# Optimization experiments

Measured on AMD Instinct MI355X. Metric: run time of the kernel, lower is better.

Reference implementation:

```python
import jax, jax.numpy as jnp
import numpy as np

N, M, DIM, OUT_DIM = 50000, 512, 256, 256
NEG = -1e9


def setup_inputs() -> dict:
    key = jax.random.key(0)
    k1, k2, k3, k4, k5, k6 = jax.random.split(key, 6)
    node_features = jax.random.normal(k1, (N, DIM), dtype=jnp.float32)
    # each node assigned to one molecule (sorted segment ids)
    mol_ids = jnp.sort(jax.random.randint(k2, (N,), 0, M))
    mol_node_matrix = (mol_ids[None, :] == jnp.arange(M)[:, None]).astype(jnp.float32)  # [M, N]
    mol_node_mask = jnp.where(mol_node_matrix > 0, 0.0, NEG).astype(jnp.float32)  # [M, N]
    # Linear params (PyTorch-style uniform init)
    bound = 1.0 / np.sqrt(DIM)
    W_attend = jax.random.uniform(k3, (DIM, OUT_DIM), minval=-bound, maxval=bound, dtype=jnp.float32)
    b_attend = jax.random.uniform(k4, (OUT_DIM,), minval=-bound, maxval=bound, dtype=jnp.float32)
    w_align = jax.random.uniform(k5, (DIM, 1), minval=-bound, maxval=bound, dtype=jnp.float32)
    b_align = jax.random.uniform(k6, (1,), minval=-bound, maxval=bound, dtype=jnp.float32)
    return {"node_features": node_features, "mol_node_matrix": mol_node_matrix,
            "mol_node_mask": mol_node_mask, "W_attend": W_attend, "b_attend": b_attend,
            "w_align": w_align, "b_align": b_align}


def reference(node_features, mol_node_matrix, mol_node_mask, W_attend, b_attend, w_align, b_align):
    # h = LeakyReLU(attend(x)) : [N, out_dim]
    h = jax.nn.leaky_relu(node_features @ W_attend + b_attend, negative_slope=0.01)
    # a = align(x) : [N]  (dropout p=0 -> identity)
    a = (node_features @ w_align + b_align)[:, 0]
    # mol_node_matrix @ diag(a) == mol_node_matrix * a[None, :]  (same math, no NxN diag)
    logits = mol_node_matrix * a[None, :] + mol_node_mask  # [M, N]
    mol_node_weight = jax.nn.softmax(logits, axis=1)
    return mol_node_weight @ h, mol_node_weight
```

## Files before the change

kernel.cpp:

```cpp
#include <hip/hip_runtime.h>
#include <cstdint>
#include <cstddef>

#define N_NODES 50000
#define M_MOLS  512
#define DIMK    256
#define ODIM    256

#define NCH   99
#define CW    32
#define NSAMP (NCH * CW)
#define NGAP  (NCH - 1)

#define NB_WPACK 32
#define K0_GRID  (NCH + NB_WPACK)

#define NB_ALIGN 1563
#define K1_GRID  (NGAP + NCH + 1 + NB_ALIGN)

#define POOL_BLOCKS 512
#define WPB   4
#define QPB   3125
#define NB_WRITE (M_MOLS * WPB)
#define K2_GRID  (POOL_BLOCKS + NB_WRITE)
#define NF4   (N_NODES / 4)
#define A_CAP 1024

typedef float  f32x4  __attribute__((ext_vector_type(4)));
typedef __bf16 bf16x8 __attribute__((ext_vector_type(8)));

static __device__ __forceinline__ short f2bf(float f) {
  unsigned u = __builtin_bit_cast(unsigned, f);
  u = u + 0x7fffu + ((u >> 16) & 1u);
  return (short)(u >> 16);
}

static __device__ __forceinline__ int chunk_base(int c) {
  return (c < NCH - 1) ? c * 512 : (N_NODES - CW);
}

__global__ __launch_bounds__(256) void k_prep(
    const float* __restrict__ mat, const float* __restrict__ W,
    int* __restrict__ smolid, int4* __restrict__ wp) {
  int b = blockIdx.x, t = threadIdx.x;
  if (b < NCH) {
    int base = chunk_base(b);
    int cp = (t & 15) * 2;
    int rg = t >> 4;
    int idx = -1, idy = -1;
    const float* p0 = mat + (size_t)(rg * 32) * N_NODES + base + cp;
#pragma unroll 16
    for (int r = 0; r < 32; r++) {
      float2 v = *(const float2*)(p0 + (size_t)r * N_NODES);
      if (v.x != 0.f) idx = rg * 32 + r;
      if (v.y != 0.f) idy = rg * 32 + r;
    }
    __shared__ int sm[16][32];
    sm[rg][cp] = idx; sm[rg][cp + 1] = idy;
    __syncthreads();
    if (t < 32) {
      int best = -1;
#pragma unroll
      for (int g = 0; g < 16; g++) best = max(best, sm[g][t]);
      smolid[b * CW + t] = best;
    }
  } else {
    int g  = (b - NCH) * 256 + t;
    int l  = g & 63;
    int Ju = g >> 6;
    int J  = Ju >> 3, u = Ju & 7;
    int j  = J * 16 + (l & 15);
    int k0 = u * 32 + (l >> 4) * 8;
    short sv[8];
#pragma unroll
    for (int i = 0; i < 8; i++) sv[i] = f2bf(W[(size_t)(k0 + i) * ODIM + j]);
    wp[Ju * 64 + l] = *(int4*)sv;
  }
}

__global__ __launch_bounds__(256) void k_bal(
    const float* __restrict__ x, const float* __restrict__ mat,
    const float* __restrict__ wa, const float* __restrict__ ba,
    const int* __restrict__ smolid, int* __restrict__ strt,
    float* __restrict__ a) {
  int b = blockIdx.x, t = threadIdx.x;
  if (b < NGAP) {
    int p  = chunk_base(b) + CW - 1;
    int q  = chunk_base(b + 1);
    int ag = smolid[b * CW + CW - 1];
    int bg = smolid[(b + 1) * CW];
    if (bg == ag) return;
    int Wd = q - p;
    int nr = bg - ag;
    __shared__ int f1[512];
    int wave = t >> 6, l = t & 63;
    for (int rr = wave; rr < nr; rr += 4) {
      const float* rp = mat + (size_t)(ag + 1 + rr) * N_NODES + p + 1;
      int mn = 0x7fffffff;
      for (int i = l; i < Wd; i += 64)
        if (rp[i] != 0.f) { mn = i; break; }
#pragma unroll
      for (int o = 1; o < 64; o <<= 1) mn = min(mn, __shfl_xor(mn, o));
      if (l == 0) f1[rr] = mn;
    }
    __syncthreads();
    if (t == 0) {
      int run = 0x7fffffff;
      for (int rr = nr - 1; rr >= 0; rr--) {
        run = min(run, f1[rr]);
        strt[ag + 1 + rr] = p + 1 + run;
      }
    }
  } else if (b < NGAP + NCH) {
    int cc = b - NGAP;
    if (t >= 1 && t < CW) {
      int prev = smolid[cc * CW + t - 1], cur = smolid[cc * CW + t];
      int col = chunk_base(cc) + t;
      for (int m = prev + 1; m <= cur; m++) strt[m] = col;
    }
  } else if (b == NGAP + NCH) {
    int first = smolid[0], last = smolid[NSAMP - 1];
    for (int m = t; m <= M_MOLS; m += 256) {
      if (m <= first) strt[m] = 0;
      else if (m > last) strt[m] = N_NODES;
    }
  } else {
    int tid = (b - NGAP - NCH - 1) * 256 + t;
    int row = tid >> 3, sub = tid & 7;
    if (row >= N_NODES) return;
    const float4* xr = (const float4*)(x + (size_t)row * DIMK) + sub * 8;
    const float4* wr = (const float4*)wa + sub * 8;
    float s = 0.f;
#pragma unroll
    for (int i = 0; i < 8; i++) {
      float4 xv = xr[i], wv = wr[i];
      s += xv.x * wv.x + xv.y * wv.y + xv.z * wv.z + xv.w * wv.w;
    }
    s += __shfl_xor(s, 1); s += __shfl_xor(s, 2); s += __shfl_xor(s, 4);
    if (sub == 0) a[row] = s + ba[0];
  }
}

__global__ __launch_bounds__(256, 2) void k_out(
    const float* __restrict__ x, const float* __restrict__ a,
    const int* __restrict__ strt, const int4* __restrict__ wp,
    const float* __restrict__ bias, float* __restrict__ out0,
    float* __restrict__ out1) {
  int b = blockIdx.x;
  int t = threadIdx.x;

  if (b >= POOL_BLOCKS) {
    int wb = b - POOL_BLOCKS;
    int m = wb >> 2, quarter = wb & 3;
    int s = strt[m], e = strt[m + 1];
    int s4 = s >> 2, e4 = (e + 3) >> 2;
    float4* orow = (float4*)out1 + (size_t)m * NF4;
    int q0 = quarter * QPB, q1 = q0 + QPB;
    float4 z; z.x = z.y = z.z = z.w = 0.f;
    for (int q = q0 + t; q < q1; q += 256)
      if (q < s4 || q >= e4) orow[q] = z;
    return;
  }

  int m = b;
  int seg_s = strt[m], seg_e = strt[m + 1];
  int L = seg_e - seg_s;

  __shared__ float a_lds[A_CAP];
  __shared__ __align__(16) short xs[16 * 256];
  __shared__ float fred[4];

  for (int i = t; i < L; i += 256) a_lds[i] = a[seg_s + i];
  __syncthreads();
  float mx = -3e38f;
  for (int i = t; i < L; i += 256) mx = fmaxf(mx, a_lds[i]);
#pragma unroll
  for (int o = 1; o < 64; o <<= 1) mx = fmaxf(mx, __shfl_xor(mx, o));
  if ((t & 63) == 0) fred[t >> 6] = mx;
  __syncthreads();
  mx = fmaxf(fmaxf(fred[0], fred[1]), fmaxf(fred[2], fred[3]));
  __syncthreads();
  float sm = 0.f;
  for (int i = t; i < L; i += 256) sm += __expf(a_lds[i] - mx);
#pragma unroll
  for (int o = 1; o < 64; o <<= 1) sm += __shfl_xor(sm, o);
  if ((t & 63) == 0) fred[t >> 6] = sm;
  __syncthreads();
  sm = fred[0] + fred[1] + fred[2] + fred[3];
  float inv = (sm > 0.f) ? 1.f / sm : 0.f;
  for (int i = t; i < L; i += 256) a_lds[i] = __expf(a_lds[i] - mx) * inv;
  __syncthreads();

  {
    int s4 = seg_s >> 2, e4 = (seg_e + 3) >> 2;
    float4* orow = (float4*)out1 + (size_t)m * NF4;
    for (int q = s4 + t; q < e4; q += 256) {
      int n = q * 4;
      float4 o;
      o.x = (n     >= seg_s && n     < seg_e) ? a_lds[n     - seg_s] : 0.f;
      o.y = (n + 1 >= seg_s && n + 1 < seg_e) ? a_lds[n + 1 - seg_s] : 0.f;
      o.z = (n + 2 >= seg_s && n + 2 < seg_e) ? a_lds[n + 2 - seg_s] : 0.f;
      o.w = (n + 3 >= seg_s && n + 3 < seg_e) ? a_lds[n + 3 - seg_s] : 0.f;
      orow[q] = o;
    }
  }

  int wave = t >> 6, l = t & 63;
  bf16x8 wfrag[4][8];
#pragma unroll
  for (int t2 = 0; t2 < 4; t2++)
#pragma unroll
    for (int u = 0; u < 8; u++)
      wfrag[t2][u] = __builtin_bit_cast(bf16x8, wp[((wave * 4 + t2) * 8 + u) * 64 + l]);
  float bias_r[4];
#pragma unroll
  for (int t2 = 0; t2 < 4; t2++) bias_r[t2] = bias[wave * 64 + t2 * 16 + (l & 15)];

  float pooled[4] = {0.f, 0.f, 0.f, 0.f};
  int r = l & 15, g = l >> 4;
  int swr = (r & 7) << 4;
  char* lb = (char*)xs;

  int nt2 = (L + 15) >> 4;
  for (int tile = 0; tile < nt2; tile++) {
    int base = seg_s + tile * 16;
    __syncthreads();
    {
      int row = t >> 4;
      int c0  = (t & 15) * 16;
      int n   = base + row;
      short sv[16];
      if (n < seg_e) {
        const float4* src = (const float4*)(x + (size_t)n * DIMK + c0);
        float4 A = src[0], B = src[1], C = src[2], D = src[3];
        sv[0]  = f2bf(A.x); sv[1]  = f2bf(A.y); sv[2]  = f2bf(A.z); sv[3]  = f2bf(A.w);
        sv[4]  = f2bf(B.x); sv[5]  = f2bf(B.y); sv[6]  = f2bf(B.z); sv[7]  = f2bf(B.w);
        sv[8]  = f2bf(C.x); sv[9]  = f2bf(C.y); sv[10] = f2bf(C.z); sv[11] = f2bf(C.w);
        sv[12] = f2bf(D.x); sv[13] = f2bf(D.y); sv[14] = f2bf(D.z); sv[15] = f2bf(D.w);
      } else {
#pragma unroll
        for (int i = 0; i < 16; i++) sv[i] = 0;
      }
      int sw = (row & 7) << 4;
      *(int4*)(lb + (row << 9) + (((c0 << 1)     ) ^ sw)) = *(int4*)(sv);
      *(int4*)(lb + (row << 9) + (((c0 << 1) + 16) ^ sw)) = *(int4*)(sv + 8);
    }
    __syncthreads();
    bf16x8 af[8];
#pragma unroll
    for (int u = 0; u < 8; u++)
      af[u] = __builtin_bit_cast(bf16x8,
                *(const int4*)(lb + (r << 9) + (((u << 6) + (g << 4)) ^ swr)));
#pragma unroll
    for (int t2 = 0; t2 < 4; t2++) {
      f32x4 acc = {0.f, 0.f, 0.f, 0.f};
#pragma unroll
      for (int u = 0; u < 8; u++)
        acc = __builtin_amdgcn_mfma_f32_16x16x32_bf16(af[u], wfrag[t2][u], acc, 0, 0, 0);
      float p = 0.f;
#pragma unroll
      for (int i = 0; i < 4; i++) {
        int ridx = tile * 16 + (g << 2) + i;
        float wgt = (ridx < L) ? a_lds[ridx] : 0.f;
        float h = acc[i] + bias_r[t2];
        h = h > 0.f ? h : 0.01f * h;
        p += wgt * h;
      }
      pooled[t2] += p;
    }
  }
#pragma unroll
  for (int t2 = 0; t2 < 4; t2++) {
    float p = pooled[t2];
    p += __shfl_xor(p, 16);
    p += __shfl_xor(p, 32);
    pooled[t2] = p;
  }
  if (l < 16) {
#pragma unroll
    for (int t2 = 0; t2 < 4; t2++)
      out0[m * ODIM + wave * 64 + t2 * 16 + l] = pooled[t2];
  }
}

extern "C" void kernel_launch(void* const* d_in, const int* in_sizes, int n_in,
                              void* d_out, int out_size, void* d_ws, size_t ws_size,
                              hipStream_t stream) {
  const float* x   = (const float*)d_in[0];
  const float* mat = (const float*)d_in[1];
  const float* W   = (const float*)d_in[3];
  const float* bA  = (const float*)d_in[4];
  const float* wa  = (const float*)d_in[5];
  const float* ba  = (const float*)d_in[6];

  float* out0 = (float*)d_out;
  float* out1 = out0 + (size_t)M_MOLS * ODIM;

  char*  ws     = (char*)d_ws;
  float* a      = (float*)(ws);
  int*   smolid = (int*)  (ws + 200064);
  int*   strt   = (int*)  (ws + 212800);
  int4*  wp     = (int4*) (ws + 215040);

  k_prep<<<K0_GRID, 256, 0, stream>>>(mat, W, smolid, wp);
  k_bal <<<K1_GRID, 256, 0, stream>>>(x, mat, wa, ba, smolid, strt, a);
  k_out <<<K2_GRID, 256, 0, stream>>>(x, a, strt, wp, bA, out0, out1);
}
```

Before: 52.92 us.

## Split pooling into node-parallel GEMM, softmax stats, and weighted-sum kernels

```diff
diff --git a/kernel.cpp b/kernel.cpp
--- a/kernel.cpp
+++ b/kernel.cpp
@@ -14,17 +14,18 @@
 
 #define NB_WPACK 32
 #define K0_GRID  (NCH + NB_WPACK)
-
-#define NB_ALIGN 1563
-#define K1_GRID  (NGAP + NCH + 1 + NB_ALIGN)
-
-#define POOL_BLOCKS 512
+#define K1_GRID  (NGAP + NCH + 1)
+
+#define HG_ROWS 64
+#define NB_HG   ((N_NODES + HG_ROWS - 1) / HG_ROWS)
+#define NTILE   (N_NODES / 16)
+
+#define POOL_BLOCKS 1024
 #define WPB   4
 #define QPB   3125
-#define NB_WRITE (M_MOLS * WPB)
-#define K2_GRID  (POOL_BLOCKS + NB_WRITE)
+#define K4_GRID (POOL_BLOCKS + M_MOLS * WPB)
 #define NF4   (N_NODES / 4)
-#define A_CAP 1024
+#define A_CAP 512
 
 typedef float  f32x4  __attribute__((ext_vector_type(4)));
 typedef __bf16 bf16x8 __attribute__((ext_vector_type(8)));
@@ -33,6 +34,13 @@
   unsigned u = __builtin_bit_cast(unsigned, f);
   u = u + 0x7fffu + ((u >> 16) & 1u);
   return (short)(u >> 16);
+}
+static __device__ __forceinline__ float bf2f(short s) {
+  unsigned u = ((unsigned)(unsigned short)s) << 16;
+  return __builtin_bit_cast(float, u);
+}
+static __device__ __forceinline__ float dot4(float4 a, float4 b) {
+  return a.x * b.x + a.y * b.y + a.z * b.z + a.w * b.w;
 }
 
 static __device__ __forceinline__ int chunk_base(int c) {
@@ -78,11 +86,9 @@
   }
 }
 
-__global__ __launch_bounds__(256) void k_bal(
-    const float* __restrict__ x, const float* __restrict__ mat,
-    const float* __restrict__ wa, const float* __restrict__ ba,
-    const int* __restrict__ smolid, int* __restrict__ strt,
-    float* __restrict__ a) {
+__global__ __launch_bounds__(256) void k_bnd(
+    const float* __restrict__ mat, const int* __restrict__ smolid,
+    int* __restrict__ strt) {
   int b = blockIdx.x, t = threadIdx.x;
   if (b < NGAP) {
     int p  = chunk_base(b) + CW - 1;
@@ -118,94 +124,23 @@
       int col = chunk_base(cc) + t;
       for (int m = prev + 1; m <= cur; m++) strt[m] = col;
     }
-  } else if (b == NGAP + NCH) {
+  } else {
     int first = smolid[0], last = smolid[NSAMP - 1];
     for (int m = t; m <= M_MOLS; m += 256) {
       if (m <= first) strt[m] = 0;
       else if (m > last) strt[m] = N_NODES;
     }
-  } else {
-    int tid = (b - NGAP - NCH - 1) * 256 + t;
-    int row = tid >> 3, sub = tid & 7;
-    if (row >= N_NODES) return;
-    const float4* xr = (const float4*)(x + (size_t)row * DIMK) + sub * 8;
-    const float4* wr = (const float4*)wa + sub * 8;
-    float s = 0.f;
-#pragma unroll
-    for (int i = 0; i < 8; i++) {
-      float4 xv = xr[i], wv = wr[i];
-      s += xv.x * wv.x + xv.y * wv.y + xv.z * wv.z + xv.w * wv.w;
-    }
-    s += __shfl_xor(s, 1); s += __shfl_xor(s, 2); s += __shfl_xor(s, 4);
-    if (sub == 0) a[row] = s + ba[0];
-  }
-}
-
-__global__ __launch_bounds__(256, 2) void k_out(
-    const float* __restrict__ x, const float* __restrict__ a,
-    const int* __restrict__ strt, const int4* __restrict__ wp,
-    const float* __restrict__ bias, float* __restrict__ out0,
-    float* __restrict__ out1) {
-  int b = blockIdx.x;
-  int t = threadIdx.x;
-
-  if (b >= POOL_BLOCKS) {
-    int wb = b - POOL_BLOCKS;
-    int m = wb >> 2, quarter = wb & 3;
-    int s = strt[m], e = strt[m + 1];
-    int s4 = s >> 2, e4 = (e + 3) >> 2;
-    float4* orow = (float4*)out1 + (size_t)m * NF4;
-    int q0 = quarter * QPB, q1 = q0 + QPB;
-    float4 z; z.x = z.y = z.z = z.w = 0.f;
-    for (int q = q0 + t; q < q1; q += 256)
-      if (q < s4 || q >= e4) orow[q] = z;
-    return;
-  }
-
-  int m = b;
-  int seg_s = strt[m], seg_e = strt[m + 1];
-  int L = seg_e - seg_s;
-
-  __shared__ float a_lds[A_CAP];
-  __shared__ __align__(16) short xs[16 * 256];
-  __shared__ float fred[4];
-
-  for (int i = t; i < L; i += 256) a_lds[i] = a[seg_s + i];
-  __syncthreads();
-  float mx = -3e38f;
-  for (int i = t; i < L; i += 256) mx = fmaxf(mx, a_lds[i]);
-#pragma unroll
-  for (int o = 1; o < 64; o <<= 1) mx = fmaxf(mx, __shfl_xor(mx, o));
-  if ((t & 63) == 0) fred[t >> 6] = mx;
-  __syncthreads();
-  mx = fmaxf(fmaxf(fred[0], fred[1]), fmaxf(fred[2], fred[3]));
-  __syncthreads();
-  float sm = 0.f;
-  for (int i = t; i < L; i += 256) sm += __expf(a_lds[i] - mx);
-#pragma unroll
-  for (int o = 1; o < 64; o <<= 1) sm += __shfl_xor(sm, o);
-  if ((t & 63) == 0) fred[t >> 6] = sm;
-  __syncthreads();
-  sm = fred[0] + fred[1] + fred[2] + fred[3];
-  float inv = (sm > 0.f) ? 1.f / sm : 0.f;
-  for (int i = t; i < L; i += 256) a_lds[i] = __expf(a_lds[i] - mx) * inv;
-  __syncthreads();
-
-  {
-    int s4 = seg_s >> 2, e4 = (seg_e + 3) >> 2;
-    float4* orow = (float4*)out1 + (size_t)m * NF4;
-    for (int q = s4 + t; q < e4; q += 256) {
-      int n = q * 4;
-      float4 o;
-      o.x = (n     >= seg_s && n     < seg_e) ? a_lds[n     - seg_s] : 0.f;
-      o.y = (n + 1 >= seg_s && n + 1 < seg_e) ? a_lds[n + 1 - seg_s] : 0.f;
-      o.z = (n + 2 >= seg_s && n + 2 < seg_e) ? a_lds[n + 2 - seg_s] : 0.f;
-      o.w = (n + 3 >= seg_s && n + 3 < seg_e) ? a_lds[n + 3 - seg_s] : 0.f;
-      orow[q] = o;
-    }
-  }
-
+  }
+}
+
+__global__ __launch_bounds__(256) void k_hgemm(
+    const float* __restrict__ x, const float* __restrict__ wa,
+    const float* __restrict__ ba, const int4* __restrict__ wp,
+    const float* __restrict__ bias, float* __restrict__ a,
+    short* __restrict__ hw) {
+  int b = blockIdx.x, t = threadIdx.x;
   int wave = t >> 6, l = t & 63;
+
   bf16x8 wfrag[4][8];
 #pragma unroll
   for (int t2 = 0; t2 < 4; t2++)
@@ -216,23 +151,32 @@
 #pragma unroll
   for (int t2 = 0; t2 < 4; t2++) bias_r[t2] = bias[wave * 64 + t2 * 16 + (l & 15)];
 
-  float pooled[4] = {0.f, 0.f, 0.f, 0.f};
-  int r = l & 15, g = l >> 4;
-  int swr = (r & 7) << 4;
+  int srow = t >> 4, c0 = (t & 15) * 16;
+  float4 wa_loc[4];
+  {
+    const float4* wr = (const float4*)wa + (c0 >> 2);
+#pragma unroll
+    for (int i = 0; i < 4; i++) wa_loc[i] = wr[i];
+  }
+  float ba0 = ba[0];
+
+  __shared__ __align__(16) short xs[16 * 256];
   char* lb = (char*)xs;
-
-  int nt2 = (L + 15) >> 4;
-  for (int tile = 0; tile < nt2; tile++) {
-    int base = seg_s + tile * 16;
+  int r = l & 15, g = l >> 4, swr = (r & 7) << 4;
+  int sw = (srow & 7) << 4;
+
+  for (int tile = 0; tile < 4; ++tile) {
+    int n0 = b * HG_ROWS + tile * 16;
+    int n  = n0 + srow;
     __syncthreads();
     {
-      int row = t >> 4;
-      int c0  = (t & 15) * 16;
-      int n   = base + row;
       short sv[16];
-      if (n < seg_e) {
+      float pa = 0.f;
+      if (n < N_NODES) {
         const float4* src = (const float4*)(x + (size_t)n * DIMK + c0);
         float4 A = src[0], B = src[1], C = src[2], D = src[3];
+        pa = dot4(A, wa_loc[0]) + dot4(B, wa_loc[1]) +
+             dot4(C, wa_loc[2]) + dot4(D, wa_loc[3]);
         sv[0]  = f2bf(A.x); sv[1]  = f2bf(A.y); sv[2]  = f2bf(A.z); sv[3]  = f2bf(A.w);
         sv[4]  = f2bf(B.x); sv[5]  = f2bf(B.y); sv[6]  = f2bf(B.z); sv[7]  = f2bf(B.w);
         sv[8]  = f2bf(C.x); sv[9]  = f2bf(C.y); sv[10] = f2bf(C.z); sv[11] = f2bf(C.w);
@@ -241,45 +185,127 @@
 #pragma unroll
         for (int i = 0; i < 16; i++) sv[i] = 0;
       }
-      int sw = (row & 7) << 4;
-      *(int4*)(lb + (row << 9) + (((c0 << 1)     ) ^ sw)) = *(int4*)(sv);
-      *(int4*)(lb + (row << 9) + (((c0 << 1) + 16) ^ sw)) = *(int4*)(sv + 8);
-    }
-    __syncthreads();
+      *(int4*)(lb + (srow << 9) + (((c0 << 1)     ) ^ sw)) = *(int4*)(sv);
+      *(int4*)(lb + (srow << 9) + (((c0 << 1) + 16) ^ sw)) = *(int4*)(sv + 8);
+      pa += __shfl_xor(pa, 1); pa += __shfl_xor(pa, 2);
+      pa += __shfl_xor(pa, 4); pa += __shfl_xor(pa, 8);
+      if ((t & 15) == 0 && n < N_NODES) a[n] = pa + ba0;
+    }
+    __syncthreads();
+    if (n0 >= N_NODES) continue;
     bf16x8 af[8];
 #pragma unroll
     for (int u = 0; u < 8; u++)
       af[u] = __builtin_bit_cast(bf16x8,
                 *(const int4*)(lb + (r << 9) + (((u << 6) + (g << 4)) ^ swr)));
+    int tadr = (n0 >> 4) * 256;
 #pragma unroll
     for (int t2 = 0; t2 < 4; t2++) {
       f32x4 acc = {0.f, 0.f, 0.f, 0.f};
 #pragma unroll
       for (int u = 0; u < 8; u++)
         acc = __builtin_amdgcn_mfma_f32_16x16x32_bf16(af[u], wfrag[t2][u], acc, 0, 0, 0);
-      float p = 0.f;
+      short hv[4];
 #pragma unroll
       for (int i = 0; i < 4; i++) {
-        int ridx = tile * 16 + (g << 2) + i;
-        float wgt = (ridx < L) ? a_lds[ridx] : 0.f;
         float h = acc[i] + bias_r[t2];
         h = h > 0.f ? h : 0.01f * h;
-        p += wgt * h;
+        hv[i] = f2bf(h);
       }
-      pooled[t2] += p;
-    }
-  }
-#pragma unroll
-  for (int t2 = 0; t2 < 4; t2++) {
-    float p = pooled[t2];
-    p += __shfl_xor(p, 16);
-    p += __shfl_xor(p, 32);
-    pooled[t2] = p;
-  }
-  if (l < 16) {
-#pragma unroll
-    for (int t2 = 0; t2 < 4; t2++)
-      out0[m * ODIM + wave * 64 + t2 * 16 + l] = pooled[t2];
+      int j = wave * 64 + t2 * 16 + (l & 15);
+      *(short4*)(hw + (size_t)(tadr + j) * 16 + g * 4) = *(short4*)hv;
+    }
+  }
+}
+
+__global__ __launch_bounds__(256) void k_stats(
+    const float* __restrict__ a, const int* __restrict__ strt,
+    float* __restrict__ wval) {
+  int m = blockIdx.x, t = threadIdx.x;
+  int s = strt[m], e = strt[m + 1];
+
+  float mx = -3e38f;
+  for (int i = s + t; i < e; i += 256) mx = fmaxf(mx, a[i]);
+#pragma unroll
+  for (int o = 1; o < 64; o <<= 1) mx = fmaxf(mx, __shfl_xor(mx, o));
+  __shared__ float r0[4];
+  if ((t & 63) == 0) r0[t >> 6] = mx;
+  __syncthreads();
+  mx = fmaxf(fmaxf(r0[0], r0[1]), fmaxf(r0[2], r0[3]));
+
+  float sm = 0.f;
+  for (int i = s + t; i < e; i += 256) sm += __expf(a[i] - mx);
+#pragma unroll
+  for (int o = 1; o < 64; o <<= 1) sm += __shfl_xor(sm, o);
+  __shared__ float r1[4];
+  if ((t & 63) == 0) r1[t >> 6] = sm;
+  __syncthreads();
+  sm = r1[0] + r1[1] + r1[2] + r1[3];
+  float inv = (sm > 0.f) ? 1.f / sm : 0.f;
+
+  for (int i = s + t; i < e; i += 256) wval[i] = __expf(a[i] - mx) * inv;
+}
+
+__global__ __launch_bounds__(256) void k_out(
+    const short* __restrict__ hw, const float* __restrict__ wval,
+    const int* __restrict__ strt, float* __restrict__ out0,
+    float* __restrict__ out1) {
+  int b = blockIdx.x, t = threadIdx.x;
+
+  if (b < POOL_BLOCKS) {
+    int m = b >> 1, jh = b & 1;
+    int s = strt[m], e = strt[m + 1];
+    int L = e - s;
+    __shared__ float wl[A_CAP];
+    for (int i = t; i < L; i += 256) wl[i] = wval[s + i];
+    __syncthreads();
+    float acc = 0.f;
+    if (L > 0) {
+      int j = jh * 128 + (t & 127);
+      int half = t >> 7;
+      int t0 = s >> 4, t1 = (e - 1) >> 4;
+      for (int tt = t0 + half; tt <= t1; tt += 2) {
+        const int4* hp = (const int4*)(hw + (size_t)(tt * 256 + j) * 16);
+        int4 lo = hp[0], hi = hp[1];
+        int base = tt * 16 - s;
+        const short* ls = (const short*)&lo;
+        const short* hs = (const short*)&hi;
+#pragma unroll
+        for (int k = 0; k < 8; k++) {
+          int rr = base + k;
+          float wt = ((unsigned)rr < (unsigned)L) ? wl[rr] : 0.f;
+          acc += wt * bf2f(ls[k]);
+        }
+#pragma unroll
+        for (int k = 0; k < 8; k++) {
+          int rr = base + 8 + k;
+          float wt = ((unsigned)rr < (unsigned)L) ? wl[rr] : 0.f;
+          acc += wt * bf2f(hs[k]);
+        }
+      }
+    }
+    __shared__ float pr[256];
+    pr[t] = acc;
+    __syncthreads();
+    if (t < 128) out0[m * ODIM + jh * 128 + t] = pr[t] + pr[t + 128];
+    return;
+  }
+
+  int wb = b - POOL_BLOCKS;
+  int m = wb >> 2, quarter = wb & 3;
+  int s = strt[m], e = strt[m + 1];
+  const float4* wv4 = (const float4*)wval;
+  float4* orow = (float4*)out1 + (size_t)m * NF4;
+  int q0 = quarter * QPB, q1 = q0 + QPB;
+  for (int q = q0 + t; q < q1; q += 256) {
+    int n = q * 4;
+    float4 w = wv4[q];
+    float4 o;
+    o.x = ((unsigned)(n     - s) < (unsigned)(e - s)) ? w.x : 0.f;
+    o.y = ((unsigned)(n + 1 - s) < (unsigned)(e - s)) ? w.y : 0.f;
+    o.z = ((unsigned)(n + 2 - s) < (unsigned)(e - s)) ? w.z : 0.f;
+    o.w = ((unsigned)(n + 3 - s) < (unsigned)(e - s)) ? w.w : 0.f;
+    orow[q] = o;
   }
 }
 
@@ -300,9 +326,13 @@
   float* a      = (float*)(ws);
   int*   smolid = (int*)  (ws + 200064);
   int*   strt   = (int*)  (ws + 212800);
-  int4*  wp     = (int4*) (ws + 215040);
-
-  k_prep<<<K0_GRID, 256, 0, stream>>>(mat, W, smolid, wp);
-  k_bal <<<K1_GRID, 256, 0, stream>>>(x, mat, wa, ba, smolid, strt, a);
-  k_out <<<K2_GRID, 256, 0, stream>>>(x, a, strt, wp, bA, out0, out1);
-}
+  float* wval   = (float*)(ws + 214912);
+  int4*  wp     = (int4*) (ws + 414912);
+  short* hw     = (short*)(ws + 557056);
+
+  k_prep <<<K0_GRID, 256, 0, stream>>>(mat, W, smolid, wp);
+  k_bnd  <<<K1_GRID, 256, 0, stream>>>(mat, smolid, strt);
+  k_hgemm<<<NB_HG,   256, 0, stream>>>(x, wa, ba, wp, bA, a, hw);
+  k_stats<<<M_MOLS,  256, 0, stream>>>(a, strt, wval);
+  k_out  <<<K4_GRID, 256, 0, stream>>>(hw, wval, strt, out0, out1);
+}
```

Measured after the change: 58.20 us. 10.0% more time.
